# Optimization experiments

Measured on AMD Instinct MI355X. Metric: run time of the kernel, lower is better.

Reference implementation:

```python
import jax, jax.numpy as jnp
import numpy as np
from jax import lax

VOCAB = 32000
D = 256      # d_model
N = 16       # n_neurons
NL = 6       # n_layers
DS = 16      # d_state
DC = 4       # d_conv
DI = 512     # d_inner = expand * d_model
DTR = 16     # dt_rank = ceil(D/16)
NH = 4       # attention heads
HD = D // NH
B, L = 1, 128


def setup_inputs() -> dict:
    key = jax.random.key(0)
    ks = list(jax.random.split(key, 32))
    it = iter(ks)

    def rn(shape, scale):
        return jax.random.normal(next(it), shape, jnp.float32) * scale

    p = {}
    p["x"] = jax.random.randint(next(it), (B, L), 0, VOCAB, dtype=jnp.int32)
    p["embedding"] = rn((VOCAB, D), 0.02)
    p["norm1_w"] = jnp.ones((NL, D)); p["norm1_b"] = jnp.zeros((NL, D))
    p["norm2_w"] = jnp.ones((NL, D)); p["norm2_b"] = jnp.zeros((NL, D))
    # Mamba params (stacked over layers)
    p["in_proj_w"] = rn((NL, 2 * DI, D), D ** -0.5)
    p["conv_w"] = rn((NL, DI, DC), DC ** -0.5)
    p["conv_b"] = jnp.zeros((NL, DI))
    p["x_proj_w"] = rn((NL, DTR + 2 * DS, DI), DI ** -0.5)
    p["dt_proj_w"] = rn((NL, DI, DTR), DTR ** -0.5)
    dt0 = jax.random.uniform(next(it), (NL, DI), jnp.float32, 1e-3, 1e-1)
    p["dt_proj_b"] = jnp.log(jnp.expm1(dt0))  # inverse softplus init
    p["A_log"] = jnp.log(jnp.tile(jnp.arange(1.0, DS + 1.0, dtype=jnp.float32), (NL, DI, 1)))
    p["skip_D"] = jnp.ones((NL, DI))
    p["out_proj_w"] = rn((NL, D, DI), DI ** -0.5)
    # cross-neuron MHA params
    p["attn_in_w"] = rn((NL, 3 * D, D), D ** -0.5)
    p["attn_in_b"] = jnp.zeros((NL, 3 * D))
    p["attn_out_w"] = rn((NL, D, D), D ** -0.5)
    p["attn_out_b"] = jnp.zeros((NL, D))
    p["norm_f_w"] = jnp.ones((D,)); p["norm_f_b"] = jnp.zeros((D,))
    p["head_b"] = jnp.zeros((VOCAB,))
    return p


def _ln(x, w, b):
    m = x.mean(-1, keepdims=True)
    v = ((x - m) ** 2).mean(-1, keepdims=True)
    return (x - m) * lax.rsqrt(v + 1e-5) * w + b


def _mamba(x, ipw, cw, cb, xpw, dpw, dpb, alog, dskip, opw):
    # x: (BN, L, D)
    BN, Ls, _ = x.shape
    xz = x @ ipw.T                       # (BN, L, 2*DI)
    u, z = xz[..., :DI], xz[..., DI:]
    # depthwise causal conv1d, kernel DC, left-pad DC-1
    uc = lax.conv_general_dilated(
        u.swapaxes(1, 2), cw[:, None, :], (1,), [(DC - 1, 0)],
        dimension_numbers=("NCH", "OIH", "NCH"), feature_group_count=DI)
    u = jax.nn.silu(uc + cb[None, :, None]).swapaxes(1, 2)  # (BN, L, DI)
    xdbl = u @ xpw.T                     # (BN, L, DTR+2*DS)
    dt = jax.nn.softplus(xdbl[..., :DTR] @ dpw.T + dpb)     # (BN, L, DI)
    Bm = xdbl[..., DTR:DTR + DS]
    Cm = xdbl[..., DTR + DS:]
    A = -jnp.exp(alog)                   # (DI, DS)

    def step(h, ins):
        dt_t, b_t, c_t, u_t = ins        # (BN,DI) (BN,DS) (BN,DS) (BN,DI)
        h = jnp.exp(dt_t[..., None] * A) * h + (dt_t * u_t)[..., None] * b_t[:, None, :]
        return h, jnp.einsum("bds,bs->bd", h, c_t)

    h0 = jnp.zeros((BN, DI, DS), x.dtype)
    _, ys = lax.scan(step, h0, (dt.swapaxes(0, 1), Bm.swapaxes(0, 1),
                                Cm.swapaxes(0, 1), u.swapaxes(0, 1)))
    y = ys.swapaxes(0, 1) + u * dskip
    return (y * jax.nn.silu(z)) @ opw.T


def _mha(x, iw, ib, ow, ob):
    # x: (B*L, N, D); self-attention across neurons
    Bq, S, _ = x.shape
    qkv = x @ iw.T + ib
    q, k, v = jnp.split(qkv, 3, axis=-1)
    q = q.reshape(Bq, S, NH, HD); k = k.reshape(Bq, S, NH, HD); v = v.reshape(Bq, S, NH, HD)
    att = jax.nn.softmax(jnp.einsum("bqhd,bkhd->bhqk", q, k) / np.float32(np.sqrt(HD)), axis=-1)
    o = jnp.einsum("bhqk,bkhd->bqhd", att, v).reshape(Bq, S, D)
    return o @ ow.T + ob


def reference(x, embedding, norm1_w, norm1_b, norm2_w, norm2_b, in_proj_w, conv_w,
              conv_b, x_proj_w, dt_proj_w, dt_proj_b, A_log, skip_D, out_proj_w,
              attn_in_w, attn_in_b, attn_out_w, attn_out_b, norm_f_w, norm_f_b, head_b):
    Bb, Ll = x.shape
    h = embedding[x]                                             # (B, L, D)
    h = jnp.broadcast_to(h[:, None], (Bb, N, Ll, D)).reshape(Bb * N, Ll, D)
    for i in range(NL):
        h = h + _mamba(_ln(h, norm1_w[i], norm1_b[i]), in_proj_w[i], conv_w[i],
                       conv_b[i], x_proj_w[i], dt_proj_w[i], dt_proj_b[i],
                       A_log[i], skip_D[i], out_proj_w[i])
        xc = _ln(h, norm2_w[i], norm2_b[i]).reshape(Bb, N, Ll, D)
        xc = xc.transpose(0, 2, 1, 3).reshape(Bb * Ll, N, D)
        co = _mha(xc, attn_in_w[i], attn_in_b[i], attn_out_w[i], attn_out_b[i])
        h = h + co.reshape(Bb, Ll, N, D).transpose(0, 2, 1, 3).reshape(Bb * N, Ll, D)
    h = h.reshape(Bb, N, Ll, D).mean(axis=1)                     # avg over neurons
    return _ln(h, norm_f_w, norm_f_b) @ embedding.T + head_b     # tied head
```

## Files before the change

kernel.cpp:

```cpp
#include <hip/hip_runtime.h>

constexpr int SEQ    = 128;
constexpr int NVOCAB = 32000;

constexpr size_t O_HA = 0;
constexpr size_t O_HB = O_HA + (size_t)SEQ*256;
constexpr size_t O_U  = O_HB + (size_t)SEQ*256;
constexpr size_t O_DT = O_U  + (size_t)SEQ*512;
constexpr size_t O_ZS = O_DT + (size_t)SEQ*512;
constexpr size_t O_BC = O_ZS + (size_t)SEQ*512;
constexpr size_t O_YG = O_BC + (size_t)SEQ*32;
constexpr size_t O_AH = O_YG + (size_t)SEQ*512;
constexpr size_t O_WC = O_AH + (size_t)SEQ*256;
constexpr size_t O_BB = O_WC + (size_t)6*256*256;

__device__ __forceinline__ float wsum(float p) {
    #pragma unroll
    for (int m = 1; m < 64; m <<= 1) p += __shfl_xor(p, m);
    return p;
}
__device__ __forceinline__ float dot4(float4 a, float4 b) {
    return a.x*b.x + a.y*b.y + a.z*b.z + a.w*b.w;
}

__global__ __launch_bounds__(256) void combo_kernel(
    const float* __restrict__ aiw, const float* __restrict__ aib,
    const float* __restrict__ aow, const float* __restrict__ aob,
    float* __restrict__ wc, float* __restrict__ bc)
{
    __shared__ float sA[32*68];
    __shared__ float sB[32*68];
    const int l  = blockIdx.x >> 4;
    const int t  = blockIdx.x & 15;
    const int r0 = (t >> 2) * 64;
    const int n0 = (t & 3) * 64;
    const int tid = threadIdx.x;

    const float* av = aiw + (size_t)l*768*256 + (size_t)512*256;
    const float* ab = aib + l*768 + 512;
    const float* ow = aow + (size_t)l*256*256;
    const float* ob = aob + l*256;

    const int ar = tid & 63, ah = (tid >> 6) * 8;
    const int bk = tid >> 3, bn = (tid & 7) * 8;
    const float* Ap = ow + (size_t)(r0 + ar)*256 + ah;
    const float* Bp = av + (size_t)bk*256 + n0 + bn;

    const int rg = tid >> 4, cg = tid & 15;

    float4 ra0 = *(const float4*)(Ap);
    float4 ra1 = *(const float4*)(Ap + 4);
    float4 rb0 = *(const float4*)(Bp);
    float4 rb1 = *(const float4*)(Bp + 4);

    float acc[4][4] = {};

    for (int kc = 0; kc < 256; kc += 32) {
        if (kc) __syncthreads();
        sA[(ah+0)*68+ar]=ra0.x; sA[(ah+1)*68+ar]=ra0.y; sA[(ah+2)*68+ar]=ra0.z; sA[(ah+3)*68+ar]=ra0.w;
        sA[(ah+4)*68+ar]=ra1.x; sA[(ah+5)*68+ar]=ra1.y; sA[(ah+6)*68+ar]=ra1.z; sA[(ah+7)*68+ar]=ra1.w;
        *(float4*)&sB[bk*68+bn]   = rb0;
        *(float4*)&sB[bk*68+bn+4] = rb1;
        __syncthreads();
        if (kc + 32 < 256) {
            ra0 = *(const float4*)(Ap + kc + 32);
            ra1 = *(const float4*)(Ap + kc + 36);
            rb0 = *(const float4*)(Bp + (size_t)(kc + 32)*256);
            rb1 = *(const float4*)(Bp + (size_t)(kc + 32)*256 + 4);
        }
        #pragma unroll
        for (int k = 0; k < 32; ++k) {
            float4 a = *(const float4*)&sA[k*68 + rg*4];
            float4 b = *(const float4*)&sB[k*68 + cg*4];
            acc[0][0] += a.x*b.x; acc[0][1] += a.x*b.y; acc[0][2] += a.x*b.z; acc[0][3] += a.x*b.w;
            acc[1][0] += a.y*b.x; acc[1][1] += a.y*b.y; acc[1][2] += a.y*b.z; acc[1][3] += a.y*b.w;
            acc[2][0] += a.z*b.x; acc[2][1] += a.z*b.y; acc[2][2] += a.z*b.z; acc[2][3] += a.z*b.w;
            acc[3][0] += a.w*b.x; acc[3][1] += a.w*b.y; acc[3][2] += a.w*b.z; acc[3][3] += a.w*b.w;
        }
    }

    float* wout = wc + (size_t)l*256*256;
    #pragma unroll
    for (int i = 0; i < 4; ++i) {
        int row = r0 + rg*4 + i;
        float4 o; o.x = acc[i][0]; o.y = acc[i][1]; o.z = acc[i][2]; o.w = acc[i][3];
        *(float4*)&wout[(size_t)row*256 + n0 + cg*4] = o;
    }

    if (n0 == 0 && tid < 64) {
        int c = r0 + tid;
        float b = ob[c];
        for (int j0 = 0; j0 < 256; j0 += 4) {
            float4 a4 = *(const float4*)&ow[(size_t)c*256 + j0];
            float4 b4 = *(const float4*)&ab[j0];
            b += dot4(a4, b4);
        }
        bc[l*256 + c] = b;
    }
}

template<int MR, int KK, int S>
__device__ __forceinline__ void gemm3(
    const float* __restrict__ Wg, const float* __restrict__ A, int AS,
    float* __restrict__ dest, int DS,
    const float* __restrict__ addsrc, int ASS, const float* __restrict__ bias)
{
    constexpr int NST = KK / (4 * S);
    const int tid = threadIdx.x;
    const int tq  = tid & (S - 1);
    const int c0  = (tid / S) * 2;
    const float* Wp0 = Wg + (size_t)c0*KK + tq*4;
    const float* Wp1 = Wp0 + KK;

    float acc0[MR], acc1[MR];
    #pragma unroll
    for (int r = 0; r < MR; ++r) { acc0[r] = 0.f; acc1[r] = 0.f; }

    float4 wa0 = *(const float4*)(Wp0);
    float4 wa1 = *(const float4*)(Wp1);
    float4 wb0 = *(const float4*)(Wp0 + 4*S);
    float4 wb1 = *(const float4*)(Wp1 + 4*S);

    #pragma unroll 1
    for (int st = 0; st < NST; st += 2) {
        float4 na0, na1, nb0, nb1;
        const bool pa = (st + 2 < NST);
        const bool pb = (st + 3 < NST);
        if (pa) { na0 = *(const float4*)(Wp0 + (st+2)*4*S);
                  na1 = *(const float4*)(Wp1 + (st+2)*4*S); }
        if (pb) { nb0 = *(const float4*)(Wp0 + (st+3)*4*S);
                  nb1 = *(const float4*)(Wp1 + (st+3)*4*S); }
        const int k0 = st*4*S + tq*4;
        #pragma unroll
        for (int r = 0; r < MR; ++r) {
            float4 a = *(const float4*)&A[r*AS + k0];
            acc0[r] += dot4(a, wa0);
            acc1[r] += dot4(a, wa1);
        }
        const int k1 = k0 + 4*S;
        #pragma unroll
        for (int r = 0; r < MR; ++r) {
            float4 a = *(const float4*)&A[r*AS + k1];
            acc0[r] += dot4(a, wb0);
            acc1[r] += dot4(a, wb1);
        }
        if (pa) { wa0 = na0; wa1 = na1; }
        if (pb) { wb0 = nb0; wb1 = nb1; }
    }
    #pragma unroll
    for (int m = 1; m < S; m <<= 1) {
        #pragma unroll
        for (int r = 0; r < MR; ++r) {
            acc0[r] += __shfl_xor(acc0[r], m);
            acc1[r] += __shfl_xor(acc1[r], m);
        }
    }
    if (tq == 0) {
        #pragma unroll
        for (int r = 0; r < MR; ++r) {
            float ox = acc0[r], oy = acc1[r];
            if (bias) { ox += bias[c0]; oy += bias[c0+1]; }
            if (addsrc) {
                float2 s = *(const float2*)&addsrc[r*ASS + c0];
                ox += s.x; oy += s.y;
            }
            float2 o; o.x = ox; o.y = oy;
            *(float2*)&dest[r*DS + c0] = o;
        }
    }
}

__device__ __forceinline__ void ln_row(const float* __restrict__ src, float* __restrict__ dst,
                                       const float* __restrict__ w, const float* __restrict__ b)
{
    int lane = threadIdx.x & 63;
    float4 x = *(const float4*)&src[lane*4];
    float sm = wsum(x.x + x.y + x.z + x.w);
    float mean = sm * (1.0f/256.0f);
    float d0 = x.x-mean, d1 = x.y-mean, d2 = x.z-mean, d3 = x.w-mean;
    float var = wsum(d0*d0 + d1*d1 + d2*d2 + d3*d3) * (1.0f/256.0f);
    float rstd = rsqrtf(var + 1e-5f);
    float4 ww = *(const float4*)&w[lane*4];
    float4 bb = *(const float4*)&b[lane*4];
    float4 o;
    o.x = d0*rstd*ww.x + bb.x;
    o.y = d1*rstd*ww.y + bb.y;
    o.z = d2*rstd*ww.z + bb.z;
    o.w = d3*rstd*ww.w + bb.w;
    *(float4*)&dst[lane*4] = o;
}

__global__ __launch_bounds__(1024, 4) void rowk_kernel(
    const int* __restrict__ x, const float* __restrict__ emb,
    const float* __restrict__ n1w_l, const float* __restrict__ n1b_l,
    const float* __restrict__ n2w_l, const float* __restrict__ n2b_l,
    const float* __restrict__ ipw_l, const float* __restrict__ cw_l, const float* __restrict__ cb_l,
    const float* __restrict__ xpw_l, const float* __restrict__ dpw_l, const float* __restrict__ dpb_l,
    const float* __restrict__ opw_l, const float* __restrict__ wc_l, const float* __restrict__ bc_l,
    const float* __restrict__ nfw, const float* __restrict__ nfb,
    const float* __restrict__ hin, float* __restrict__ hout,
    const float* __restrict__ ygv, float* __restrict__ uv, float* __restrict__ dtv,
    float* __restrict__ zsv, float* __restrict__ bcv, float* __restrict__ AH,
    int li)
{
    __shared__ float SM[6336];
    float* hP  = SM;
    float* h1  = SM + 1056;
    float* sLN = SM + 2112;
    float* sAX = SM + 3168;
    float* zR  = SM + 5248;
    float* suR = SM + 5760;
    float* sxR = SM + 6272;

    const int r = blockIdx.x;
    const int tid = threadIdx.x;
    const int lane = tid & 63, wv = tid >> 6;
    int rr[4];
    #pragma unroll
    for (int j = 0; j < 4; ++j) { int v = r - 3 + j; rr[j] = v < 0 ? 0 : v; }

    {
        int hr = tid >> 8, hc = tid & 255;
        if (li <= 1) hP[hr*264 + hc] = emb[(size_t)x[rr[hr]]*256 + hc];
        else         hP[hr*264 + hc] = hin[rr[hr]*256 + hc];
    }
    if (li >= 1) {
        int yr = tid >> 9, yc = tid & 511;
        sAX[yr*520 + yc]     = ygv[rr[yr]*512 + yc];
        sAX[(2+yr)*520 + yc] = ygv[rr[2+yr]*512 + yc];
    }
    __syncthreads();

    float* hC = hP;
    if (li >= 1) {
        gemm3<4,512,8>(opw_l, sAX, 520, h1, 264, hP, 264, nullptr);
        __syncthreads();
        if (wv < 4) ln_row(h1 + wv*264, sLN + wv*264, n2w_l, n2b_l);
        __syncthreads();
        gemm3<4,256,8>(wc_l, sLN, 264, h1, 264, h1, 264, bc_l);
        __syncthreads();
        hC = h1;
        if (tid < 256) hout[r*256 + tid] = h1[3*264 + tid];
        if (li == 6) {
            if (tid < 256) {
                float v = h1[3*264 + tid];
                float s = wsum(v);
                float q = wsum(v*v);
                if (lane == 0) { sxR[wv] = s; sxR[8 + wv] = q; }
            }
            __syncthreads();
            if (tid < 256) {
                float v = h1[3*264 + tid];
                float mean = (sxR[0]+sxR[1]+sxR[2]+sxR[3]) * (1.0f/256.0f);
                float var  = (sxR[8]+sxR[9]+sxR[10]+sxR[11]) * (1.0f/256.0f) - mean*mean;
                float rstd = rsqrtf(var + 1e-5f);
                AH[r*256 + tid] = (v - mean)*rstd*nfw[tid] + nfb[tid];
            }
            return;
        }
    }

    if (wv < 4) ln_row(hC + wv*264, sLN + wv*264, n1w_l, n1b_l);
    __syncthreads();
    gemm3<4,256,4>(ipw_l,                   sLN,         264, sAX, 520, nullptr, 0, nullptr);
    gemm3<1,256,4>(ipw_l + (size_t)512*256, sLN + 3*264, 264, zR,  512, nullptr, 0, nullptr);
    __syncthreads();

    if (tid < 512) {
        int d = tid;
        float4 c4 = *(const float4*)&cw_l[d*4];
        float acc = cb_l[d];
        if (r >= 3) acc += sAX[d]        * c4.x;
        if (r >= 2) acc += sAX[520 + d]  * c4.y;
        if (r >= 1) acc += sAX[1040 + d] * c4.z;
        acc += sAX[1560 + d] * c4.w;
        float sg = acc / (1.0f + __expf(-acc));
        suR[d] = sg;
        uv[r*512 + d] = sg;
        float z = zR[d];
        zsv[r*512 + d] = z / (1.0f + __expf(-z));
    }
    __syncthreads();

    {
        float4 a0 = *(const float4*)&suR[lane*4];
        float4 a1 = *(const float4*)&suR[256 + lane*4];
        float p[3];
        #pragma unroll
        for (int j = 0; j < 3; ++j) {
            int c = wv*3 + j;
            float4 q0 = *(const float4*)&xpw_l[(size_t)c*512 + lane*4];
            float4 q1 = *(const float4*)&xpw_l[(size_t)c*512 + 256 + lane*4];
            p[j] = dot4(a0, q0) + dot4(a1, q1);
        }
        #pragma unroll
        for (int m = 1; m < 64; m <<= 1) {
            #pragma unroll
            for (int j = 0; j < 3; ++j) p[j] += __shfl_xor(p[j], m);
        }
        if (lane == 0) {
            #pragma unroll
            for (int j = 0; j < 3; ++j) sxR[wv*3 + j] = p[j];
        }
    }
    __syncthreads();
    if (tid >= 16 && tid < 48) bcv[r*32 + tid - 16] = sxR[tid];

    if (tid < 512) {
        int d = tid;
        float4 sx0 = *(const float4*)&sxR[0];
        float4 sx1 = *(const float4*)&sxR[4];
        float4 sx2 = *(const float4*)&sxR[8];
        float4 sx3 = *(const float4*)&sxR[12];
        const float4* dp = (const float4*)&dpw_l[(size_t)d*16];
        float acc = dpb_l[d] + dot4(dp[0], sx0) + dot4(dp[1], sx1)
                             + dot4(dp[2], sx2) + dot4(dp[3], sx3);
        dtv[r*512 + d] = fmaxf(acc, 0.0f) + log1pf(__expf(-fabsf(acc)));
    }
}

__global__ __launch_bounds__(128) void scan_kernel(
    const float* __restrict__ dt, const float* __restrict__ u, const float* __restrict__ zs,
    const float* __restrict__ bcv,
    const float* __restrict__ alog_l, const float* __restrict__ dsk_l,
    float* __restrict__ yg)
{
    __shared__ float sdt[8*132];
    __shared__ float su2[8*132];
    __shared__ float sz2[8*132];
    __shared__ float sB [16*132];
    __shared__ float sC [16*132];
    const int tid = threadIdx.x;
    const int s  = tid & 15;
    const int dl = tid >> 4;
    const int d0 = blockIdx.x * 8;
    const int d  = d0 + dl;

    {
        const int t = tid;
        float4 q0, q1;
        q0 = *(const float4*)&dt[t*512 + d0];
        q1 = *(const float4*)&dt[t*512 + d0 + 4];
        sdt[0*132+t]=q0.x; sdt[1*132+t]=q0.y; sdt[2*132+t]=q0.z; sdt[3*132+t]=q0.w;
        sdt[4*132+t]=q1.x; sdt[5*132+t]=q1.y; sdt[6*132+t]=q1.z; sdt[7*132+t]=q1.w;
        q0 = *(const float4*)&u[t*512 + d0];
        q1 = *(const float4*)&u[t*512 + d0 + 4];
        su2[0*132+t]=q0.x; su2[1*132+t]=q0.y; su2[2*132+t]=q0.z; su2[3*132+t]=q0.w;
        su2[4*132+t]=q1.x; su2[5*132+t]=q1.y; su2[6*132+t]=q1.z; su2[7*132+t]=q1.w;
        q0 = *(const float4*)&zs[t*512 + d0];
        q1 = *(const float4*)&zs[t*512 + d0 + 4];
        sz2[0*132+t]=q0.x; sz2[1*132+t]=q0.y; sz2[2*132+t]=q0.z; sz2[3*132+t]=q0.w;
        sz2[4*132+t]=q1.x; sz2[5*132+t]=q1.y; sz2[6*132+t]=q1.z; sz2[7*132+t]=q1.w;
        float4 b0 = *(const float4*)&bcv[t*32 + 0];
        float4 b1 = *(const float4*)&bcv[t*32 + 4];
        float4 b2 = *(const float4*)&bcv[t*32 + 8];
        float4 b3 = *(const float4*)&bcv[t*32 + 12];
        sB[ 0*132+t]=b0.x; sB[ 1*132+t]=b0.y; sB[ 2*132+t]=b0.z; sB[ 3*132+t]=b0.w;
        sB[ 4*132+t]=b1.x; sB[ 5*132+t]=b1.y; sB[ 6*132+t]=b1.z; sB[ 7*132+t]=b1.w;
        sB[ 8*132+t]=b2.x; sB[ 9*132+t]=b2.y; sB[10*132+t]=b2.z; sB[11*132+t]=b2.w;
        sB[12*132+t]=b3.x; sB[13*132+t]=b3.y; sB[14*132+t]=b3.z; sB[15*132+t]=b3.w;
        float4 c0 = *(const float4*)&bcv[t*32 + 16];
        float4 c1 = *(const float4*)&bcv[t*32 + 20];
        float4 c2 = *(const float4*)&bcv[t*32 + 24];
        float4 c3 = *(const float4*)&bcv[t*32 + 28];
        sC[ 0*132+t]=c0.x; sC[ 1*132+t]=c0.y; sC[ 2*132+t]=c0.z; sC[ 3*132+t]=c0.w;
        sC[ 4*132+t]=c1.x; sC[ 5*132+t]=c1.y; sC[ 6*132+t]=c1.z; sC[ 7*132+t]=c1.w;
        sC[ 8*132+t]=c2.x; sC[ 9*132+t]=c2.y; sC[10*132+t]=c2.z; sC[11*132+t]=c2.w;
        sC[12*132+t]=c3.x; sC[13*132+t]=c3.y; sC[14*132+t]=c3.z; sC[15*132+t]=c3.w;
    }
    __syncthreads();

    const float a_ds = -__expf(alog_l[d*16 + s]);
    const float dskv = dsk_l[d];
    float hst = 0.0f;
    #pragma unroll 8
    for (int t = 0; t < SEQ; ++t) {
        float dtvv = sdt[dl*132 + t];
        float uvv  = su2[dl*132 + t];
        hst = __expf(dtvv * a_ds) * hst + dtvv * uvv * sB[s*132 + t];
        float p = hst * sC[s*132 + t];
        p += __shfl_xor(p, 1);
        p += __shfl_xor(p, 2);
        p += __shfl_xor(p, 4);
        p += __shfl_xor(p, 8);
        if (s == 0) yg[t*512 + d] = (p + uvv * dskv) * sz2[dl*132 + t];
    }
}

__global__ __launch_bounds__(256, 1) void head_kernel(
    const float* __restrict__ AH, const float* __restrict__ emb,
    const float* __restrict__ hb, float* __restrict__ out)
{
    const int tid  = threadIdx.x;
    const int wv   = tid >> 6;
    const int lane = tid & 63;
    const int b  = blockIdx.x;
    const int cb = b % 125, rb = b / 125;
    const int r0 = rb*64 + wv*16;
    const int c  = cb*256 + lane*4;

    const float* Ap = AH  + (size_t)r0*256;
    const float* Wp = emb + (size_t)c*256;

    float4 aE[16], aO[16], wE[4], wO[4];
    float acc[16][4];
    #pragma unroll
    for (int r = 0; r < 16; ++r) {
        #pragma unroll
        for (int j = 0; j < 4; ++j) acc[r][j] = 0.f;
    }

    #pragma unroll
    for (int r = 0; r < 16; ++r) aE[r] = *(const float4*)&Ap[r*256];
    #pragma unroll
    for (int j = 0; j < 4; ++j)  wE[j] = *(const float4*)&Wp[(size_t)j*256];

    #pragma unroll 1
    for (int k = 0; k < 256; k += 8) {
        if (k + 4 < 256) {
            #pragma unroll
            for (int r = 0; r < 16; ++r) aO[r] = *(const float4*)&Ap[r*256 + k + 4];
            #pragma unroll
            for (int j = 0; j < 4; ++j)  wO[j] = *(const float4*)&Wp[(size_t)j*256 + k + 4];
        }
        #pragma unroll
        for (int r = 0; r < 16; ++r) {
            #pragma unroll
            for (int j = 0; j < 4; ++j) acc[r][j] += dot4(aE[r], wE[j]);
        }
        if (k + 8 < 256) {
            #pragma unroll
            for (int r = 0; r < 16; ++r) aE[r] = *(const float4*)&Ap[r*256 + k + 8];
            #pragma unroll
            for (int j = 0; j < 4; ++j)  wE[j] = *(const float4*)&Wp[(size_t)j*256 + k + 8];
        }
        #pragma unroll
        for (int r = 0; r < 16; ++r) {
            #pragma unroll
            for (int j = 0; j < 4; ++j) acc[r][j] += dot4(aO[r], wO[j]);
        }
    }

    float4 h4 = *(const float4*)&hb[c];
    #pragma unroll
    for (int r = 0; r < 16; ++r) {
        float4 o;
        o.x = acc[r][0] + h4.x;
        o.y = acc[r][1] + h4.y;
        o.z = acc[r][2] + h4.z;
        o.w = acc[r][3] + h4.w;
        *(float4*)&out[(size_t)(r0 + r)*NVOCAB + c] = o;
    }
}

extern "C" void kernel_launch(void* const* d_in, const int* in_sizes, int n_in,
                              void* d_out, int out_size, void* d_ws, size_t ws_size,
                              hipStream_t stream)
{
    const int*   xin = (const int*)d_in[0];
    const float* emb = (const float*)d_in[1];
    const float* n1w = (const float*)d_in[2];
    const float* n1b = (const float*)d_in[3];
    const float* n2w = (const float*)d_in[4];
    const float* n2b = (const float*)d_in[5];
    const float* ipw = (const float*)d_in[6];
    const float* cw  = (const float*)d_in[7];
    const float* cb  = (const float*)d_in[8];
    const float* xpw = (const float*)d_in[9];
    const float* dpw = (const float*)d_in[10];
    const float* dpb = (const float*)d_in[11];
    const float* alog= (const float*)d_in[12];
    const float* dsk = (const float*)d_in[13];
    const float* opw = (const float*)d_in[14];
    const float* aiw = (const float*)d_in[15];
    const float* aib = (const float*)d_in[16];
    const float* aow = (const float*)d_in[17];
    const float* aob = (const float*)d_in[18];
    const float* nfw = (const float*)d_in[19];
    const float* nfb = (const float*)d_in[20];
    const float* hb  = (const float*)d_in[21];
    float* ws  = (float*)d_ws;
    float* out = (float*)d_out;

    combo_kernel<<<96, 256, 0, stream>>>(aiw, aib, aow, aob, ws + O_WC, ws + O_BB);

    for (int i = 0; i <= 6; ++i) {
        int ka = i <= 5 ? i : 5;
        int kc = i >= 1 ? i - 1 : 0;
        const float* hin  = (i % 2 == 0) ? ws + O_HA : ws + O_HB;
        float*       hout = (i % 2 == 0) ? ws + O_HB : ws + O_HA;
        rowk_kernel<<<128, 1024, 0, stream>>>(
            xin, emb,
            n1w + ka*256, n1b + ka*256,
            n2w + kc*256, n2b + kc*256,
            ipw + (size_t)ka*1024*256, cw + (size_t)ka*512*4, cb + ka*512,
            xpw + (size_t)ka*48*512, dpw + (size_t)ka*512*16, dpb + ka*512,
            opw + (size_t)kc*256*512,
            ws + O_WC + (size_t)kc*256*256, ws + O_BB + kc*256,
            nfw, nfb,
            hin, hout,
            ws + O_YG, ws + O_U, ws + O_DT, ws + O_ZS, ws + O_BC, ws + O_AH,
            i);
        if (i <= 5)
            scan_kernel<<<64, 128, 0, stream>>>(
                ws + O_DT, ws + O_U, ws + O_ZS, ws + O_BC,
                alog + (size_t)i*512*16, dsk + i*512, ws + O_YG);
    }
    head_kernel<<<250, 256, 0, stream>>>(ws + O_AH, emb, hb, out);
}
```

Before: 587.1 us.

## Retile head GEMM for coalesced embedding loads with 4-lane K-split and shuffle reduce

```diff
diff --git a/kernel.cpp b/kernel.cpp
--- a/kernel.cpp
+++ b/kernel.cpp
@@ -387,69 +387,60 @@
     }
 }
 
-__global__ __launch_bounds__(256, 1) void head_kernel(
+__global__ __launch_bounds__(512, 2) void head_kernel(
     const float* __restrict__ AH, const float* __restrict__ emb,
     const float* __restrict__ hb, float* __restrict__ out)
 {
     const int tid  = threadIdx.x;
     const int wv   = tid >> 6;
     const int lane = tid & 63;
-    const int b  = blockIdx.x;
-    const int cb = b % 125, rb = b / 125;
-    const int r0 = rb*64 + wv*16;
-    const int c  = cb*256 + lane*4;
-
-    const float* Ap = AH  + (size_t)r0*256;
-    const float* Wp = emb + (size_t)c*256;
-
-    float4 aE[16], aO[16], wE[4], wO[4];
-    float acc[16][4];
+    const int tq   = lane & 3;
+    const int cs   = lane >> 2;
+    const int c    = blockIdx.x * 16 + cs;
+    const int r0   = wv * 16;
+
+    const float* Ap = AH  + (size_t)r0*256 + tq*4;
+    const float* Wp = emb + (size_t)c*256  + tq*4;
+
+    float  acc[16];
+    float4 aE[16], aO[16], wE, wO;
+    #pragma unroll
+    for (int r = 0; r < 16; ++r) acc[r] = 0.f;
+
+    wE = *(const float4*)(Wp);
+    #pragma unroll
+    for (int r = 0; r < 16; ++r) aE[r] = *(const float4*)(Ap + r*256);
+
+    #pragma unroll 1
+    for (int st = 0; st < 16; st += 2) {
+        if (st + 1 < 16) {
+            wO = *(const float4*)(Wp + (st+1)*16);
+            #pragma unroll
+            for (int r = 0; r < 16; ++r) aO[r] = *(const float4*)(Ap + r*256 + (st+1)*16);
+        }
+        #pragma unroll
+        for (int r = 0; r < 16; ++r) acc[r] += dot4(aE[r], wE);
+        if (st + 2 < 16) {
+            wE = *(const float4*)(Wp + (st+2)*16);
+            #pragma unroll
+            for (int r = 0; r < 16; ++r) aE[r] = *(const float4*)(Ap + r*256 + (st+2)*16);
+        }
+        if (st + 1 < 16) {
+            #pragma unroll
+            for (int r = 0; r < 16; ++r) acc[r] += dot4(aO[r], wO);
+        }
+    }
+
     #pragma unroll
     for (int r = 0; r < 16; ++r) {
-        #pragma unroll
-        for (int j = 0; j < 4; ++j) acc[r][j] = 0.f;
-    }
-
-    #pragma unroll
-    for (int r = 0; r < 16; ++r) aE[r] = *(const float4*)&Ap[r*256];
-    #pragma unroll
-    for (int j = 0; j < 4; ++j)  wE[j] = *(const float4*)&Wp[(size_t)j*256];
-
-    #pragma unroll 1
-    for (int k = 0; k < 256; k += 8) {
-        if (k + 4 < 256) {
-            #pragma unroll
-            for (int r = 0; r < 16; ++r) aO[r] = *(const float4*)&Ap[r*256 + k + 4];
-            #pragma unroll
-            for (int j = 0; j < 4; ++j)  wO[j] = *(const float4*)&Wp[(size_t)j*256 + k + 4];
-        }
-        #pragma unroll
-        for (int r = 0; r < 16; ++r) {
-            #pragma unroll
-            for (int j = 0; j < 4; ++j) acc[r][j] += dot4(aE[r], wE[j]);
-        }
-        if (k + 8 < 256) {
-            #pragma unroll
-            for (int r = 0; r < 16; ++r) aE[r] = *(const float4*)&Ap[r*256 + k + 8];
-            #pragma unroll
-            for (int j = 0; j < 4; ++j)  wE[j] = *(const float4*)&Wp[(size_t)j*256 + k + 8];
-        }
-        #pragma unroll
-        for (int r = 0; r < 16; ++r) {
-            #pragma unroll
-            for (int j = 0; j < 4; ++j) acc[r][j] += dot4(aO[r], wO[j]);
-        }
-    }
-
-    float4 h4 = *(const float4*)&hb[c];
-    #pragma unroll
-    for (int r = 0; r < 16; ++r) {
-        float4 o;
-        o.x = acc[r][0] + h4.x;
-        o.y = acc[r][1] + h4.y;
-        o.z = acc[r][2] + h4.z;
-        o.w = acc[r][3] + h4.w;
-        *(float4*)&out[(size_t)(r0 + r)*NVOCAB + c] = o;
+        acc[r] += __shfl_xor(acc[r], 1);
+        acc[r] += __shfl_xor(acc[r], 2);
+    }
+    if (tq == 0) {
+        float b = hb[c];
+        #pragma unroll
+        for (int r = 0; r < 16; ++r)
+            out[(size_t)(r0 + r)*NVOCAB + c] = acc[r] + b;
     }
 }
 
@@ -506,5 +497,5 @@
                 ws + O_DT, ws + O_U, ws + O_ZS, ws + O_BC,
                 alog + (size_t)i*512*16, dsk + i*512, ws + O_YG);
     }
-    head_kernel<<<250, 256, 0, stream>>>(ws + O_AH, emb, hb, out);
-}
+    head_kernel<<<2000, 512, 0, stream>>>(ws + O_AH, emb, hb, out);
+}
```

Result: slower. 650.8 us (+10.9%).
